# Optimization experiments

Measured on AMD Instinct MI355X. Metric: run time of the kernel, lower is better.

## Reference

```python
import jax, jax.numpy as jnp
import numpy as np

COMMITMENT_COST = 0.25


def setup_inputs() -> dict:
    key = jax.random.key(0)
    k1, k2 = jax.random.split(key)
    B, T, D = 32, 256, 512
    K = 8192
    x = jax.random.normal(k1, (B, T, D), dtype=jnp.float32)
    # nn.Embedding init: uniform(-1/K, 1/K)
    embeddings = jax.random.uniform(k2, (K, D), dtype=jnp.float32,
                                    minval=-1.0 / K, maxval=1.0 / K)
    return {"x": x, "embeddings": embeddings}


def reference(x, embeddings):
    orig_shape = x.shape
    D = orig_shape[-1]
    x_flat = x.reshape(-1, D)                      # [N, D]

    # squared Euclidean distances via expansion (argmin-equivalent to cdist)
    x_sq = jnp.sum(x_flat * x_flat, axis=1, keepdims=True)     # [N, 1]
    e_sq = jnp.sum(embeddings * embeddings, axis=1)            # [K]
    dots = jnp.einsum('nd,kd->nk', x_flat, embeddings)         # [N, K]
    distances = x_sq - 2.0 * dots + e_sq[None, :]              # [N, K]

    indices = jnp.argmin(distances, axis=1)                    # [N]
    quantized = embeddings[indices].reshape(orig_shape)        # [..., D]
    indices = indices.reshape(orig_shape[:-1])

    commitment_loss = jnp.mean((x - jax.lax.stop_gradient(quantized)) ** 2) * COMMITMENT_COST
    codebook_loss = jnp.mean((quantized - jax.lax.stop_gradient(x)) ** 2)
    total_loss = commitment_loss + codebook_loss

    # straight-through estimator
    quantized_st = x + jax.lax.stop_gradient(quantized - x)
    return quantized_st, indices, commitment_loss, codebook_loss, total_loss
```

## Files before the change

### kernel.cpp

```cpp
#include <hip/hip_runtime.h>

#define N_ROWS 8192
#define K_CODES 8192
#define D_DIM 512

typedef unsigned long long u64;

__device__ __forceinline__ float pw_base128_sq(const float* __restrict__ p) {
  float r0 = __fmul_rn(p[0], p[0]);
  float r1 = __fmul_rn(p[1], p[1]);
  float r2 = __fmul_rn(p[2], p[2]);
  float r3 = __fmul_rn(p[3], p[3]);
  float r4 = __fmul_rn(p[4], p[4]);
  float r5 = __fmul_rn(p[5], p[5]);
  float r6 = __fmul_rn(p[6], p[6]);
  float r7 = __fmul_rn(p[7], p[7]);
  for (int i = 8; i < 128; i += 8) {
    r0 = __fadd_rn(r0, __fmul_rn(p[i + 0], p[i + 0]));
    r1 = __fadd_rn(r1, __fmul_rn(p[i + 1], p[i + 1]));
    r2 = __fadd_rn(r2, __fmul_rn(p[i + 2], p[i + 2]));
    r3 = __fadd_rn(r3, __fmul_rn(p[i + 3], p[i + 3]));
    r4 = __fadd_rn(r4, __fmul_rn(p[i + 4], p[i + 4]));
    r5 = __fadd_rn(r5, __fmul_rn(p[i + 5], p[i + 5]));
    r6 = __fadd_rn(r6, __fmul_rn(p[i + 6], p[i + 6]));
    r7 = __fadd_rn(r7, __fmul_rn(p[i + 7], p[i + 7]));
  }
  return __fadd_rn(__fadd_rn(__fadd_rn(r0, r1), __fadd_rn(r2, r3)),
                   __fadd_rn(__fadd_rn(r4, r5), __fadd_rn(r6, r7)));
}

__device__ __forceinline__ float pw_sq_512(const float* __restrict__ p) {
  float b0 = pw_base128_sq(p);
  float b1 = pw_base128_sq(p + 128);
  float b2 = pw_base128_sq(p + 256);
  float b3 = pw_base128_sq(p + 384);
  return __fadd_rn(__fadd_rn(b0, b1), __fadd_rn(b2, b3));
}

__global__ __launch_bounds__(256) void vq_sq(const float* __restrict__ x,
                                             const float* __restrict__ emb,
                                             float* __restrict__ x_sq,
                                             float* __restrict__ e_sq) {
  const int tid = blockIdx.x * 256 + threadIdx.x;
  if (tid < N_ROWS) {
    x_sq[tid] = pw_sq_512(x + tid * D_DIM);
  } else {
    const int k = tid - N_ROWS;
    e_sq[k] = pw_sq_512(emb + k * D_DIM);
  }
}

__device__ __forceinline__ void compute_chunk(const float* __restrict__ esb,
                                              const float* __restrict__ xw,
                                              int dd0, int lane,
                                              float (&acc)[8][4]) {
  const int ebase = lane * 128;
  const int lm = ((lane >> 1) & 7) ^ ((lane >> 4) & 3);
#pragma unroll
  for (int g = 0; g < 8; ++g) {
    const float* p = esb + ebase + 4 * (g ^ lm);
    const float4 ev0 = *reinterpret_cast<const float4*>(p);
    const float4 ev1 = *reinterpret_cast<const float4*>(p + 32);
    const float4 ev2 = *reinterpret_cast<const float4*>(p + 64);
    const float4 ev3 = *reinterpret_cast<const float4*>(p + 96);
#pragma unroll
    for (int r = 0; r < 8; ++r) {
      const float4 xv =
          *reinterpret_cast<const float4*>(xw + r * D_DIM + dd0 + 4 * g);
      float a0 = acc[r][0], a1 = acc[r][1], a2 = acc[r][2], a3 = acc[r][3];
      a0 = __fmaf_rn(xv.x, ev0.x, a0);
      a0 = __fmaf_rn(xv.y, ev0.y, a0);
      a0 = __fmaf_rn(xv.z, ev0.z, a0);
      a0 = __fmaf_rn(xv.w, ev0.w, a0);
      a1 = __fmaf_rn(xv.x, ev1.x, a1);
      a1 = __fmaf_rn(xv.y, ev1.y, a1);
      a1 = __fmaf_rn(xv.z, ev1.z, a1);
      a1 = __fmaf_rn(xv.w, ev1.w, a1);
      a2 = __fmaf_rn(xv.x, ev2.x, a2);
      a2 = __fmaf_rn(xv.y, ev2.y, a2);
      a2 = __fmaf_rn(xv.z, ev2.z, a2);
      a2 = __fmaf_rn(xv.w, ev2.w, a2);
      a3 = __fmaf_rn(xv.x, ev3.x, a3);
      a3 = __fmaf_rn(xv.y, ev3.y, a3);
      a3 = __fmaf_rn(xv.z, ev3.z, a3);
      a3 = __fmaf_rn(xv.w, ev3.w, a3);
      acc[r][0] = a0; acc[r][1] = a1; acc[r][2] = a2; acc[r][3] = a3;
    }
  }
}

#define STAGE1(BUF, DD0, I)                                                    \
  __builtin_amdgcn_global_load_lds(                                            \
      (const __attribute__((address_space(1))) void*)(                         \
          e + (size_t)(k0 + (t >> 3) + 64 * (I)) * D_DIM + (DD0) +             \
          4 * ((t & 7) ^ ((t >> 6) & 7) ^ ((I) & 3))),                         \
      (__attribute__((address_space(3))) void*)(&es[BUF][4 * t + 2048 * (I)]), \
      16, 0, 0)
#define STAGE(BUF, DD0)                                                        \
  do {                                                                         \
    STAGE1(BUF, DD0, 0);                                                       \
    STAGE1(BUF, DD0, 1);                                                       \
    STAGE1(BUF, DD0, 2);                                                       \
    STAGE1(BUF, DD0, 3);                                                       \
  } while (0)

__global__ __launch_bounds__(512, 4) void vq_dist(
    const float* __restrict__ x, const float* __restrict__ e,
    const float* __restrict__ x_sq, const float* __restrict__ e_sq,
    u64* __restrict__ slots) {
  __shared__ float es[2][8192];

  const int t = threadIdx.x;
  const int lane = t & 63;

  const int bx = blockIdx.x;
  const int swz = (bx & 7) * 512 + (bx >> 3);
  const int kb = swz >> 7;
  const int nb = swz & 127;
  const int k0 = kb * 256;
  const int n0w = __builtin_amdgcn_readfirstlane(nb * 64 + (t >> 6) * 8);
  const float* xw = x + (size_t)n0w * D_DIM;

  float accA[8][4], accB[8][4];
#pragma unroll
  for (int r = 0; r < 8; ++r)
#pragma unroll
    for (int j = 0; j < 4; ++j) { accA[r][j] = 0.0f; accB[r][j] = 0.0f; }

  STAGE(0, 0);
  asm volatile("s_waitcnt vmcnt(0)" ::: "memory");
  __syncthreads();

#pragma unroll 1
  for (int c = 0; c < 12; ++c) {
    STAGE((c + 1) & 1, (c + 1) * 32);
    compute_chunk(&es[c & 1][0], xw, c * 32, lane, accA);
    asm volatile("s_waitcnt vmcnt(0)" ::: "memory");
    __syncthreads();
  }
#pragma unroll 1
  for (int c = 12; c < 16; ++c) {
    if (c < 15) STAGE((c + 1) & 1, (c + 1) * 32);
    compute_chunk(&es[c & 1][0], xw, c * 32, lane, accB);
    asm volatile("s_waitcnt vmcnt(0)" ::: "memory");
    __syncthreads();
  }

  const float4 xsqa = *reinterpret_cast<const float4*>(x_sq + n0w);
  const float4 xsqb = *reinterpret_cast<const float4*>(x_sq + n0w + 4);
  const float xsq[8] = {xsqa.x, xsqa.y, xsqa.z, xsqa.w,
                        xsqb.x, xsqb.y, xsqb.z, xsqb.w};
  const int klane = k0 + lane * 4;
  const float4 esq = *reinterpret_cast<const float4*>(e_sq + klane);
  const float esqv[4] = {esq.x, esq.y, esq.z, esq.w};

#pragma unroll
  for (int r = 0; r < 8; ++r) {
    u64 best = ~0ULL;
#pragma unroll
    for (int j = 0; j < 4; ++j) {
      float dot = __fadd_rn(accA[r][j], accB[r][j]);
      float dist = __fadd_rn(__fsub_rn(xsq[r], __fmul_rn(2.0f, dot)), esqv[j]);
      unsigned int b = __float_as_uint(dist);
      unsigned int sb = (b & 0x80000000u) ? ~b : (b | 0x80000000u);
      u64 key = ((u64)sb << 32) | (unsigned)(klane + j);
      best = best < key ? best : key;
    }
#pragma unroll
    for (int off = 32; off > 0; off >>= 1) {
      u64 o = __shfl_xor((unsigned long long)best, off, 64);
      best = best < o ? best : o;
    }
    if (lane == 0) atomicMin(&slots[n0w + r], best);
  }
}

__global__ __launch_bounds__(256) void vq_out(
    const float* __restrict__ x, const float* __restrict__ e,
    const u64* __restrict__ slots, float* __restrict__ out_q,
    float* __restrict__ out_idx, double* __restrict__ loss_part) {
  const int t = threadIdx.x;
  const int w = t >> 6, lane = t & 63;
  const int n = blockIdx.x * 4 + w;
  const int idx = (int)(slots[n] & 0xFFFFFFFFULL);
  const float4* qr = (const float4*)(e + (size_t)idx * D_DIM);
  const float4* xr = (const float4*)(x + (size_t)n * D_DIM);
  float4* outr = (float4*)(out_q + (size_t)n * D_DIM);
  double s = 0.0;
#pragma unroll
  for (int i = 0; i < 2; ++i) {
    const int d4 = lane * 2 + i;
    float4 q = qr[d4];
    float4 xv = xr[d4];
    outr[d4] = q;
    double d0 = (double)xv.x - (double)q.x;
    double d1 = (double)xv.y - (double)q.y;
    double d2 = (double)xv.z - (double)q.z;
    double d3 = (double)xv.w - (double)q.w;
    s += d0 * d0 + d1 * d1 + d2 * d2 + d3 * d3;
  }
  for (int off = 32; off > 0; off >>= 1) s += __shfl_down(s, off, 64);
  if (lane == 0) {
    out_idx[n] = (float)idx;
    atomicAdd(&loss_part[(n * 37) & 255], s);
  }
}

__global__ void vq_loss(const double* __restrict__ loss_part,
                        float* __restrict__ out_s) {
  __shared__ double sm[256];
  const int t = threadIdx.x;
  sm[t] = loss_part[t];
  __syncthreads();
  for (int off = 128; off > 0; off >>= 1) {
    if (t < off) sm[t] += sm[t + off];
    __syncthreads();
  }
  if (t == 0) {
    double m = sm[0] / (double)(N_ROWS * D_DIM);
    out_s[0] = (float)(0.25 * m);
    out_s[1] = (float)m;
    out_s[2] = (float)(1.25 * m);
  }
}

extern "C" void kernel_launch(void* const* d_in, const int* in_sizes, int n_in,
                              void* d_out, int out_size, void* d_ws, size_t ws_size,
                              hipStream_t stream) {
  const float* x = (const float*)d_in[0];
  const float* emb = (const float*)d_in[1];
  float* out = (float*)d_out;

  u64* slots = (u64*)d_ws;
  float* x_sq = (float*)((char*)d_ws + 65536);
  float* e_sq = (float*)((char*)d_ws + 98304);
  double* loss_part = (double*)((char*)d_ws + 131072);

  hipMemsetAsync(d_ws, 0xFF, 65536, stream);
  hipMemsetAsync(loss_part, 0, 256 * sizeof(double), stream);

  vq_sq<<<(2 * N_ROWS) / 256, 256, 0, stream>>>(x, emb, x_sq, e_sq);
  vq_dist<<<4096, 512, 0, stream>>>(x, emb, x_sq, e_sq, slots);
  vq_out<<<N_ROWS / 4, 256, 0, stream>>>(x, emb, slots, out,
                                         out + N_ROWS * D_DIM, loss_part);
  vq_loss<<<1, 256, 0, stream>>>(loss_part, out + N_ROWS * D_DIM + N_ROWS);
}
```

Baseline: 1.026 ms.

## Halve codebook tile per block to raise occupancy in distance kernel

Measured after the change: 980.0 us. 1.05x faster.

```diff
diff --git a/kernel.cpp b/kernel.cpp
--- a/kernel.cpp
+++ b/kernel.cpp
@@ -53,21 +53,19 @@
 __device__ __forceinline__ void compute_chunk(const float* __restrict__ esb,
                                               const float* __restrict__ xw,
                                               int dd0, int lane,
-                                              float (&acc)[8][4]) {
-  const int ebase = lane * 128;
-  const int lm = ((lane >> 1) & 7) ^ ((lane >> 4) & 3);
+                                              float (&acc)[8][2]) {
+  const int rbase = lane * 64;
+  const int lm = lane & 7;
 #pragma unroll
   for (int g = 0; g < 8; ++g) {
-    const float* p = esb + ebase + 4 * (g ^ lm);
+    const float* p = esb + rbase + 4 * (g ^ lm);
     const float4 ev0 = *reinterpret_cast<const float4*>(p);
     const float4 ev1 = *reinterpret_cast<const float4*>(p + 32);
-    const float4 ev2 = *reinterpret_cast<const float4*>(p + 64);
-    const float4 ev3 = *reinterpret_cast<const float4*>(p + 96);
 #pragma unroll
     for (int r = 0; r < 8; ++r) {
       const float4 xv =
           *reinterpret_cast<const float4*>(xw + r * D_DIM + dd0 + 4 * g);
-      float a0 = acc[r][0], a1 = acc[r][1], a2 = acc[r][2], a3 = acc[r][3];
+      float a0 = acc[r][0], a1 = acc[r][1];
       a0 = __fmaf_rn(xv.x, ev0.x, a0);
       a0 = __fmaf_rn(xv.y, ev0.y, a0);
       a0 = __fmaf_rn(xv.z, ev0.z, a0);
@@ -76,15 +74,8 @@
       a1 = __fmaf_rn(xv.y, ev1.y, a1);
       a1 = __fmaf_rn(xv.z, ev1.z, a1);
       a1 = __fmaf_rn(xv.w, ev1.w, a1);
-      a2 = __fmaf_rn(xv.x, ev2.x, a2);
-      a2 = __fmaf_rn(xv.y, ev2.y, a2);
-      a2 = __fmaf_rn(xv.z, ev2.z, a2);
-      a2 = __fmaf_rn(xv.w, ev2.w, a2);
-      a3 = __fmaf_rn(xv.x, ev3.x, a3);
-      a3 = __fmaf_rn(xv.y, ev3.y, a3);
-      a3 = __fmaf_rn(xv.z, ev3.z, a3);
-      a3 = __fmaf_rn(xv.w, ev3.w, a3);
-      acc[r][0] = a0; acc[r][1] = a1; acc[r][2] = a2; acc[r][3] = a3;
+      acc[r][0] = a0;
+      acc[r][1] = a1;
     }
   }
 }
@@ -93,39 +84,38 @@
   __builtin_amdgcn_global_load_lds(                                            \
       (const __attribute__((address_space(1))) void*)(                         \
           e + (size_t)(k0 + (t >> 3) + 64 * (I)) * D_DIM + (DD0) +             \
-          4 * ((t & 7) ^ ((t >> 6) & 7) ^ ((I) & 3))),                         \
+          4 * ((t & 7) ^ ((t >> 4) & 7))),                                     \
       (__attribute__((address_space(3))) void*)(&es[BUF][4 * t + 2048 * (I)]), \
       16, 0, 0)
 #define STAGE(BUF, DD0)                                                        \
   do {                                                                         \
     STAGE1(BUF, DD0, 0);                                                       \
     STAGE1(BUF, DD0, 1);                                                       \
-    STAGE1(BUF, DD0, 2);                                                       \
-    STAGE1(BUF, DD0, 3);                                                       \
   } while (0)
 
-__global__ __launch_bounds__(512, 4) void vq_dist(
+__global__ __launch_bounds__(512, 6) void vq_dist(
     const float* __restrict__ x, const float* __restrict__ e,
     const float* __restrict__ x_sq, const float* __restrict__ e_sq,
     u64* __restrict__ slots) {
-  __shared__ float es[2][8192];
+  __shared__ float es[2][4096];
 
   const int t = threadIdx.x;
   const int lane = t & 63;
 
   const int bx = blockIdx.x;
-  const int swz = (bx & 7) * 512 + (bx >> 3);
+  const int swz = (bx & 7) * 1024 + (bx >> 3);
   const int kb = swz >> 7;
   const int nb = swz & 127;
-  const int k0 = kb * 256;
+  const int k0 = kb * 128;
   const int n0w = __builtin_amdgcn_readfirstlane(nb * 64 + (t >> 6) * 8);
   const float* xw = x + (size_t)n0w * D_DIM;
 
-  float accA[8][4], accB[8][4];
-#pragma unroll
-  for (int r = 0; r < 8; ++r)
-#pragma unroll
-    for (int j = 0; j < 4; ++j) { accA[r][j] = 0.0f; accB[r][j] = 0.0f; }
+  float accA[8][2], accB[8][2];
+#pragma unroll
+  for (int r = 0; r < 8; ++r) {
+    accA[r][0] = 0.0f; accA[r][1] = 0.0f;
+    accB[r][0] = 0.0f; accB[r][1] = 0.0f;
+  }
 
   STAGE(0, 0);
   asm volatile("s_waitcnt vmcnt(0)" ::: "memory");
@@ -150,15 +140,15 @@
   const float4 xsqb = *reinterpret_cast<const float4*>(x_sq + n0w + 4);
   const float xsq[8] = {xsqa.x, xsqa.y, xsqa.z, xsqa.w,
                         xsqb.x, xsqb.y, xsqb.z, xsqb.w};
-  const int klane = k0 + lane * 4;
-  const float4 esq = *reinterpret_cast<const float4*>(e_sq + klane);
-  const float esqv[4] = {esq.x, esq.y, esq.z, esq.w};
+  const int klane = k0 + 2 * lane;
+  const float2 esq = *reinterpret_cast<const float2*>(e_sq + klane);
+  const float esqv[2] = {esq.x, esq.y};
 
 #pragma unroll
   for (int r = 0; r < 8; ++r) {
     u64 best = ~0ULL;
 #pragma unroll
-    for (int j = 0; j < 4; ++j) {
+    for (int j = 0; j < 2; ++j) {
       float dot = __fadd_rn(accA[r][j], accB[r][j]);
       float dist = __fadd_rn(__fsub_rn(xsq[r], __fmul_rn(2.0f, dot)), esqv[j]);
       unsigned int b = __float_as_uint(dist);
@@ -240,7 +230,7 @@
   hipMemsetAsync(loss_part, 0, 256 * sizeof(double), stream);
 
   vq_sq<<<(2 * N_ROWS) / 256, 256, 0, stream>>>(x, emb, x_sq, e_sq);
-  vq_dist<<<4096, 512, 0, stream>>>(x, emb, x_sq, e_sq, slots);
+  vq_dist<<<8192, 512, 0, stream>>>(x, emb, x_sq, e_sq, slots);
   vq_out<<<N_ROWS / 4, 256, 0, stream>>>(x, emb, slots, out,
                                          out + N_ROWS * D_DIM, loss_part);
   vq_loss<<<1, 256, 0, stream>>>(loss_part, out + N_ROWS * D_DIM + N_ROWS);
```
